# Kernel tuning notes

Hardware: AMD Instinct MI355X
Metric: run time of the kernel (lower is better)

The kernel has to match this reference:

```python
import jax, jax.numpy as jnp
import numpy as np

B, S, D, H = 2, 2048, 1024, 16
HD = D // H  # 64

def setup_inputs() -> dict:
    key = jax.random.key(0)
    ks = jax.random.split(key, 6)
    s = 1.0 / np.sqrt(D)
    return {
        "x": jax.random.normal(ks[0], (B, S, D), dtype=jnp.float32),
        "wq": jax.random.normal(ks[1], (D, D), dtype=jnp.float32) * s,
        "wk": jax.random.normal(ks[2], (D, D), dtype=jnp.float32) * s,
        "wv": jax.random.normal(ks[3], (D, D), dtype=jnp.float32) * s,
        "wo": jax.random.normal(ks[4], (D, D), dtype=jnp.float32) * s,
        "bo": jax.random.normal(ks[5], (D,), dtype=jnp.float32) * 0.01,
    }

def reference(x, wq, wk, wv, wo, bo):
    b, s, _ = x.shape
    # QKV projections (qkvBias=False), reshape to [b, h, s, hd]
    q = (x @ wq).reshape(b, s, H, HD).transpose(0, 2, 1, 3)
    k = (x @ wk).reshape(b, s, H, HD).transpose(0, 2, 1, 3)
    v = (x @ wv).reshape(b, s, H, HD).transpose(0, 2, 1, 3)
    # scores, causal mask (upper triangle -> -inf), scale, softmax
    scores = jnp.einsum('bhqd,bhkd->bhqk', q, k)
    causal = jnp.triu(jnp.ones((s, s), dtype=bool), k=1)
    scores = jnp.where(causal, -jnp.inf, scores) / np.sqrt(HD)
    weights = jax.nn.softmax(scores, axis=-1)  # dropout=0 (eval)
    ctx = jnp.einsum('bhqk,bhkd->bhqd', weights, v)
    ctx = ctx.transpose(0, 2, 1, 3).reshape(b, s, D)
    return ctx @ wo + bo
```

## Files before the change

kernel.cpp:

```cpp
#include <hip/hip_runtime.h>
#include <hip/hip_bf16.h>
#include <math.h>

#define BB 2
#define SS 2048
#define DD 1024
#define HH 16
#define HDIM 64

typedef unsigned short u16;
typedef __attribute__((ext_vector_type(8))) short bfrag;
typedef __attribute__((ext_vector_type(4))) short s16x4;
typedef __attribute__((ext_vector_type(4))) float f32x4;

#define NEG_BIG (-1e30f)
#define QSCALE 0.18033688011112042f

__device__ __forceinline__ u16 f2u(float f) {
    unsigned int u = __builtin_bit_cast(unsigned int, f);
    u += 0x7fffu + ((u >> 16) & 1u);
    return (u16)(u >> 16);
}

__device__ __forceinline__ void async16(const u16* g, u16* l) {
    __builtin_amdgcn_global_load_lds((__attribute__((address_space(1))) void*)g,
                                     (__attribute__((address_space(3))) void*)l,
                                     16, 0, 0);
}

__device__ __forceinline__ f32x4 mfma16(bfrag a, bfrag b, f32x4 c) {
    return __builtin_amdgcn_mfma_f32_16x16x32_bf16(a, b, c, 0, 0, 0);
}

__device__ __forceinline__ f32x4 mfma_pv(s16x4 a, s16x4 b, f32x4 c) {
#if __has_builtin(__builtin_amdgcn_mfma_f32_16x16x16_bf16)
    return __builtin_amdgcn_mfma_f32_16x16x16_bf16(a, b, c, 0, 0, 0);
#elif __has_builtin(__builtin_amdgcn_mfma_f32_16x16x16bf16_1k)
    return __builtin_amdgcn_mfma_f32_16x16x16bf16_1k(a, b, c, 0, 0, 0);
#else
    f32x4 d;
    asm("v_mfma_f32_16x16x16_bf16 %0, %1, %2, %3" : "=v"(d) : "v"(a), "v"(b), "v"(c));
    return d;
#endif
}

__global__ __launch_bounds__(256) void prep_k(
    const float* __restrict__ x,  u16* __restrict__ xb,
    const float* __restrict__ wq, const float* __restrict__ wk,
    const float* __restrict__ wv, const float* __restrict__ wo,
    u16* __restrict__ wT)
{
    const int id = blockIdx.x;
    const int t = threadIdx.x;
    if (id < 2048) {
        int i = (id * 256 + t) * 8;
        float4 a = *(const float4*)(x + i);
        float4 b = *(const float4*)(x + i + 4);
        u16 o[8] = { f2u(a.x), f2u(a.y), f2u(a.z), f2u(a.w),
                     f2u(b.x), f2u(b.y), f2u(b.z), f2u(b.w) };
        *(uint4*)(xb + i) = *(uint4*)o;
        return;
    }
    const int wid = id - 2048;
    const int z = wid >> 8;
    const int kt = wid & 15, nt = (wid >> 4) & 15;
    const float* w = (z == 0) ? wq : (z == 1) ? wk : (z == 2) ? wv : wo;
    u16* o = wT + (size_t)z * DD * DD;
    __shared__ __align__(16) u16 T[64][72];
    const int k0 = kt * 64, n0 = nt * 64;
    {
        int kr = t >> 2, nb = (t & 3) * 16;
        const float4* s4 = (const float4*)(w + (size_t)(k0 + kr) * DD + n0 + nb);
        #pragma unroll
        for (int jj = 0; jj < 4; ++jj) {
            float4 v = s4[jj];
            T[kr][nb + jj*4 + 0] = f2u(v.x);
            T[kr][nb + jj*4 + 1] = f2u(v.y);
            T[kr][nb + jj*4 + 2] = f2u(v.z);
            T[kr][nb + jj*4 + 3] = f2u(v.w);
        }
    }
    __syncthreads();
    {
        int nr = t >> 2, kb = (t & 3) * 16;
        u16 tmp[16];
        #pragma unroll
        for (int j = 0; j < 16; ++j) tmp[j] = T[kb + j][nr];
        *(uint4*)(o + (size_t)(n0 + nr) * DD + k0 + kb)     = ((uint4*)tmp)[0];
        *(uint4*)(o + (size_t)(n0 + nr) * DD + k0 + kb + 8) = ((uint4*)tmp)[1];
    }
}

__global__ __launch_bounds__(256) void gemm_qkv_k(
    const u16* __restrict__ xb, const u16* __restrict__ wT,
    u16* __restrict__ Qo, u16* __restrict__ Ko, u16* __restrict__ Vt)
{
    const u16* wTz = wT + (size_t)blockIdx.z * DD * DD;
    const float osc = (blockIdx.z == 0) ? QSCALE : 1.0f;

    __shared__ __align__(16) u16 As[128 * 64];
    __shared__ __align__(16) u16 Bs[64 * 64];

    const int t = threadIdx.x;
    const int m0 = blockIdx.x * 128, n0 = blockIdx.y * 64;
    const int lane15 = t & 15, quad = (t >> 4) & 3, wave = t >> 6;
    const int wm = wave & 1, wn = wave >> 1;

    int arow[4], acol[4];
    #pragma unroll
    for (int i = 0; i < 4; ++i) {
        int c = t + i * 256;
        arow[i] = c >> 3;
        acol[i] = (c & 7) ^ (arow[i] & 7);
    }
    const int br0 = t >> 3,         bs0 = t & 7;
    const int br1 = (t + 256) >> 3, bs1 = (t + 256) & 7;
    const int bc0 = bs0 ^ (br0 & 7);
    const int bc1 = bs1 ^ (br1 & 7);
    const int ldb = (t & 192) * 8;

    int aoff[4][2], boff[2][2];
    #pragma unroll
    for (int mi = 0; mi < 4; ++mi) {
        int r = wm * 64 + mi * 16 + lane15;
        #pragma unroll
        for (int kh = 0; kh < 2; ++kh)
            aoff[mi][kh] = (r * 8 + ((kh * 4 + quad) ^ (r & 7))) * 8;
    }
    #pragma unroll
    for (int ni = 0; ni < 2; ++ni) {
        int r = wn * 32 + ni * 16 + lane15;
        #pragma unroll
        for (int kh = 0; kh < 2; ++kh)
            boff[ni][kh] = (r * 8 + ((kh * 4 + quad) ^ (r & 7))) * 8;
    }

    f32x4 acc[4][2];
    #pragma unroll
    for (int mi = 0; mi < 4; ++mi)
        #pragma unroll
        for (int ni = 0; ni < 2; ++ni)
            acc[mi][ni] = (f32x4){0.f, 0.f, 0.f, 0.f};

    for (int it = 0; it < 16; ++it) {
        const int k0 = it * 64;
        #pragma unroll
        for (int i = 0; i < 4; ++i)
            async16(xb + (size_t)(m0 + arow[i]) * DD + k0 + acol[i] * 8,
                    As + ldb + i * 2048);
        async16(wTz + (size_t)(n0 + br0) * DD + k0 + bc0 * 8, Bs + ldb);
        async16(wTz + (size_t)(n0 + br1) * DD + k0 + bc1 * 8, Bs + ldb + 2048);
        __syncthreads();
        #pragma unroll
        for (int kh = 0; kh < 2; ++kh) {
            bfrag av[4], bv[2];
            #pragma unroll
            for (int mi = 0; mi < 4; ++mi) av[mi] = *(const bfrag*)(As + aoff[mi][kh]);
            #pragma unroll
            for (int ni = 0; ni < 2; ++ni) bv[ni] = *(const bfrag*)(Bs + boff[ni][kh]);
            #pragma unroll
            for (int mi = 0; mi < 4; ++mi)
                #pragma unroll
                for (int ni = 0; ni < 2; ++ni)
                    acc[mi][ni] = mfma16(av[mi], bv[ni], acc[mi][ni]);
        }
        __syncthreads();
    }

    const int h = n0 >> 6;
    const int bq = m0 >> 11;
    const int ms = m0 & (SS - 1);

    if (blockIdx.z != 2) {
        u16* out = (blockIdx.z == 0) ? Qo : Ko;
        u16* dst = out + (((size_t)(bq * HH + h)) * SS) * HDIM;
        #pragma unroll
        for (int mi = 0; mi < 4; ++mi) {
            #pragma unroll
            for (int r = 0; r < 4; ++r) {
                int s = ms + wm * 64 + mi * 16 + quad * 4 + r;
                #pragma unroll
                for (int ni = 0; ni < 2; ++ni) {
                    int hd = wn * 32 + ni * 16 + lane15;
                    dst[(size_t)s * HDIM + hd] = f2u(acc[mi][ni][r] * osc);
                }
            }
        }
    } else {
        u16* T = As;
        __syncthreads();
        #pragma unroll
        for (int mi = 0; mi < 4; ++mi)
            #pragma unroll
            for (int r = 0; r < 4; ++r) {
                int ml = wm * 64 + mi * 16 + quad * 4 + r;
                #pragma unroll
                for (int ni = 0; ni < 2; ++ni) {
                    int nl = wn * 32 + ni * 16 + lane15;
                    T[nl * 128 + (ml ^ ((nl & 7) << 4))] = f2u(acc[mi][ni][r]);
                }
            }
        __syncthreads();
        u16* dst = Vt + ((size_t)(bq * HH + h)) * (HDIM * SS);
        #pragma unroll
        for (int i = 0; i < 4; ++i) {
            int c = t + i * 256;
            int row = c >> 4;
            int mb  = (c & 15) * 8;
            uint4 val = *(const uint4*)&T[row * 128 + (mb ^ ((row & 7) << 4))];
            *(uint4*)(dst + (size_t)row * SS + ms + mb) = val;
        }
    }
}

__global__ __launch_bounds__(256) void gemm_out_k(
    const u16* __restrict__ ctxb, const u16* __restrict__ woT,
    const float* __restrict__ bo, float* __restrict__ out)
{
    __shared__ __align__(16) u16 As[128 * 64];
    __shared__ __align__(16) u16 Bs[64 * 64];

    const int t = threadIdx.x;
    const int m0 = blockIdx.x * 128, n0 = blockIdx.y * 64;
    const int lane15 = t & 15, quad = (t >> 4) & 3, wave = t >> 6;
    const int wm = wave & 1, wn = wave >> 1;

    int arow[4], acol[4];
    #pragma unroll
    for (int i = 0; i < 4; ++i) {
        int c = t + i * 256;
        arow[i] = c >> 3;
        acol[i] = (c & 7) ^ (arow[i] & 7);
    }
    const int br0 = t >> 3,         bs0 = t & 7;
    const int br1 = (t + 256) >> 3, bs1 = (t + 256) & 7;
    const int bc0 = bs0 ^ (br0 & 7);
    const int bc1 = bs1 ^ (br1 & 7);
    const int ldb = (t & 192) * 8;

    int aoff[4][2], boff[2][2];
    #pragma unroll
    for (int mi = 0; mi < 4; ++mi) {
        int r = wm * 64 + mi * 16 + lane15;
        #pragma unroll
        for (int kh = 0; kh < 2; ++kh)
            aoff[mi][kh] = (r * 8 + ((kh * 4 + quad) ^ (r & 7))) * 8;
    }
    #pragma unroll
    for (int ni = 0; ni < 2; ++ni) {
        int r = wn * 32 + ni * 16 + lane15;
        #pragma unroll
        for (int kh = 0; kh < 2; ++kh)
            boff[ni][kh] = (r * 8 + ((kh * 4 + quad) ^ (r & 7))) * 8;
    }

    f32x4 acc[4][2];
    #pragma unroll
    for (int mi = 0; mi < 4; ++mi)
        #pragma unroll
        for (int ni = 0; ni < 2; ++ni)
            acc[mi][ni] = (f32x4){0.f, 0.f, 0.f, 0.f};

    for (int it = 0; it < 16; ++it) {
        const int k0 = it * 64;
        #pragma unroll
        for (int i = 0; i < 4; ++i)
            async16(ctxb + (size_t)(m0 + arow[i]) * DD + k0 + acol[i] * 8,
                    As + ldb + i * 2048);
        async16(woT + (size_t)(n0 + br0) * DD + k0 + bc0 * 8, Bs + ldb);
        async16(woT + (size_t)(n0 + br1) * DD + k0 + bc1 * 8, Bs + ldb + 2048);
        __syncthreads();
        #pragma unroll
        for (int kh = 0; kh < 2; ++kh) {
            bfrag av[4], bv[2];
            #pragma unroll
            for (int mi = 0; mi < 4; ++mi) av[mi] = *(const bfrag*)(As + aoff[mi][kh]);
            #pragma unroll
            for (int ni = 0; ni < 2; ++ni) bv[ni] = *(const bfrag*)(Bs + boff[ni][kh]);
            #pragma unroll
            for (int mi = 0; mi < 4; ++mi)
                #pragma unroll
                for (int ni = 0; ni < 2; ++ni)
                    acc[mi][ni] = mfma16(av[mi], bv[ni], acc[mi][ni]);
        }
        __syncthreads();
    }

    float bias[2];
    #pragma unroll
    for (int ni = 0; ni < 2; ++ni)
        bias[ni] = bo[n0 + wn * 32 + ni * 16 + lane15];

    #pragma unroll
    for (int mi = 0; mi < 4; ++mi) {
        #pragma unroll
        for (int r = 0; r < 4; ++r) {
            int m = m0 + wm * 64 + mi * 16 + quad * 4 + r;
            #pragma unroll
            for (int ni = 0; ni < 2; ++ni) {
                int n = n0 + wn * 32 + ni * 16 + lane15;
                out[(size_t)m * DD + n] = acc[mi][ni][r] + bias[ni];
            }
        }
    }
}

struct AttnState {
    f32x4 acc_o[4];
    f32x4 acc_s;
};

template<bool MASKED>
__device__ __forceinline__ void qkt_pv(
    const u16* __restrict__ Kc, const u16* __restrict__ Vc,
    const bfrag bq[2], const int koff[2], const int voffb[4],
    bool qhi, int kv0, int qg, int quad4,
    AttnState& st, s16x4 ones4)
{
    f32x4 sT[4];
    #pragma unroll
    for (int ni = 0; ni < 4; ++ni) sT[ni] = (f32x4){0.f, 0.f, 0.f, 0.f};

    bfrag vv[2][4];
    #pragma unroll
    for (int nd = 0; nd < 4; ++nd)
        vv[0][nd] = *(const bfrag*)&Vc[voffb[0] + nd * 1024];

    __builtin_amdgcn_s_setprio(1);
    #pragma unroll
    for (int kh = 0; kh < 2; ++kh)
        #pragma unroll
        for (int ni = 0; ni < 4; ++ni)
            sT[ni] = mfma16(*(const bfrag*)&Kc[koff[kh] + ni * 1024], bq[kh], sT[ni]);
    __builtin_amdgcn_s_setprio(0);

    #pragma unroll
    for (int ni = 0; ni < 4; ++ni) {
        if (ni < 3) {
            #pragma unroll
            for (int nd = 0; nd < 4; ++nd)
                vv[(ni + 1) & 1][nd] = *(const bfrag*)&Vc[voffb[ni + 1] + nd * 1024];
        }
        float pv[4];
        #pragma unroll
        for (int r = 0; r < 4; ++r) {
            float v = sT[ni][r];
            if (MASKED) {
                int kvg = kv0 + ni * 16 + quad4 + r;
                if (kvg > qg) v = NEG_BIG;
            }
            pv[r] = exp2f(v);
        }
        unsigned lo = __builtin_amdgcn_perm(
            __builtin_bit_cast(unsigned, pv[1]),
            __builtin_bit_cast(unsigned, pv[0]), 0x07060302u);
        unsigned hi = __builtin_amdgcn_perm(
            __builtin_bit_cast(unsigned, pv[3]),
            __builtin_bit_cast(unsigned, pv[2]), 0x07060302u);
        s16x4 pf = __builtin_bit_cast(s16x4,
            ((unsigned long long)hi << 32) | (unsigned long long)lo);
        __builtin_amdgcn_s_setprio(1);
        st.acc_s = mfma_pv(ones4, pf, st.acc_s);
        #pragma unroll
        for (int nd = 0; nd < 4; ++nd) {
            bfrag v8 = vv[ni & 1][nd];
            s16x4 vlo = __builtin_shufflevector(v8, v8, 0, 1, 2, 3);
            s16x4 vhi = __builtin_shufflevector(v8, v8, 4, 5, 6, 7);
            s16x4 va = qhi ? vhi : vlo;
            st.acc_o[nd] = mfma_pv(va, pf, st.acc_o[nd]);
        }
        __builtin_amdgcn_s_setprio(0);
    }
}

__global__ __launch_bounds__(256, 4) void attn_k(
    const u16* __restrict__ Q, const u16* __restrict__ K,
    const u16* __restrict__ Vt, u16* __restrict__ ctx)
{
    __shared__ __align__(16) u16 Ks[2][64 * 64];
    __shared__ __align__(16) u16 Vs[2][64 * 64];
    const int t = threadIdx.x;
    const int lane15 = t & 15, quad = (t >> 4) & 3, wave = t >> 6;
    const int bh = blockIdx.x;
    const int yy = (int)blockIdx.y;
    const int y0 = yy & 7, rnd = yy >> 3;
    const int qt = (rnd == 0) ? 31 - y0 : (rnd == 1) ? y0
                 : (rnd == 2) ? 23 - y0 : 8 + y0;
    const int q0 = qt * 64;
    const int b = bh >> 4, h = bh & 15;
    const u16* Qb = Q  + (size_t)bh * SS * HDIM;
    const u16* Kb = K  + (size_t)bh * SS * HDIM;
    const u16* Vb = Vt + (size_t)bh * HDIM * SS;

    const int kr0 = t >> 3,         ks0 = t & 7;
    const int kr1 = (t + 256) >> 3, ks1 = (t + 256) & 7;
    const int kc0 = ks0 ^ (kr0 & 7);
    const int kc1 = ks1 ^ (kr1 & 7);
    const int ldst = (t & 192) * 8;

    async16(Qb + (size_t)(q0 + kr0) * HDIM + kc0 * 8, &Ks[1][ldst]);
    async16(Qb + (size_t)(q0 + kr1) * HDIM + kc1 * 8, &Ks[1][ldst + 2048]);
    async16(Kb + (size_t)kr0 * HDIM + kc0 * 8, &Ks[0][ldst]);
    async16(Kb + (size_t)kr1 * HDIM + kc1 * 8, &Ks[0][ldst + 2048]);
    async16(Vb + (size_t)kr0 * SS + kc0 * 8, &Vs[0][ldst]);
    async16(Vb + (size_t)kr1 * SS + kc1 * 8, &Vs[0][ldst + 2048]);

    const int r7 = lane15 & 7;
    int koff[2];
    #pragma unroll
    for (int kh = 0; kh < 2; ++kh)
        koff[kh] = (lane15 * 8 + ((kh * 4 + quad) ^ r7)) * 8;
    int voffb[4];
    #pragma unroll
    for (int ni = 0; ni < 4; ++ni)
        voffb[ni] = (lane15 * 8 + ((ni * 2 + (quad >> 1)) ^ r7)) * 8;
    const bool qhi = (quad & 1) != 0;

    __syncthreads();
    bfrag bq[2];
    bq[0] = *(const bfrag*)&Ks[1][koff[0] + wave * 1024];
    bq[1] = *(const bfrag*)&Ks[1][koff[1] + wave * 1024];
    __syncthreads();

    s16x4 ones4;
    #pragma unroll
    for (int i = 0; i < 4; ++i) ones4[i] = (short)0x3f80;

    AttnState st;
    st.acc_s = (f32x4){0.f, 0.f, 0.f, 0.f};
    #pragma unroll
    for (int nd = 0; nd < 4; ++nd) st.acc_o[nd] = (f32x4){0.f, 0.f, 0.f, 0.f};

    const int qg = q0 + wave * 16 + lane15;
    const int quad4 = quad * 4;

    for (int kt = 0; kt < qt; ++kt) {
        const int nv0 = (kt + 1) * 64;
        const int pb = (kt + 1) & 1;
        async16(Kb + (size_t)(nv0 + kr0) * HDIM + kc0 * 8, &Ks[pb][ldst]);
        async16(Kb + (size_t)(nv0 + kr1) * HDIM + kc1 * 8, &Ks[pb][ldst + 2048]);
        async16(Vb + (size_t)kr0 * SS + nv0 + kc0 * 8, &Vs[pb][ldst]);
        async16(Vb + (size_t)kr1 * SS + nv0 + kc1 * 8, &Vs[pb][ldst + 2048]);
        qkt_pv<false>(Ks[kt & 1], Vs[kt & 1], bq, koff, voffb,
                      qhi, kt * 64, qg, quad4, st, ones4);
        __syncthreads();
    }
    qkt_pv<true>(Ks[qt & 1], Vs[qt & 1], bq, koff, voffb,
                 qhi, qt * 64, qg, quad4, st, ones4);

    const float inv = 1.f / st.acc_s[0];
    const int srow = q0 + wave * 16 + lane15;
    u16* dst = ctx + ((size_t)b * SS + srow) * DD + h * HDIM + quad4;
    #pragma unroll
    for (int nd = 0; nd < 4; ++nd) {
        uint2 stw;
        stw.x = (unsigned)f2u(st.acc_o[nd][0] * inv) |
                ((unsigned)f2u(st.acc_o[nd][1] * inv) << 16);
        stw.y = (unsigned)f2u(st.acc_o[nd][2] * inv) |
                ((unsigned)f2u(st.acc_o[nd][3] * inv) << 16);
        *(uint2*)(dst + nd * 16) = stw;
    }
}

extern "C" void kernel_launch(void* const* d_in, const int* in_sizes, int n_in,
                              void* d_out, int out_size, void* d_ws, size_t ws_size,
                              hipStream_t stream) {
    const float* x  = (const float*)d_in[0];
    const float* wq = (const float*)d_in[1];
    const float* wk = (const float*)d_in[2];
    const float* wv = (const float*)d_in[3];
    const float* wo = (const float*)d_in[4];
    const float* bo = (const float*)d_in[5];
    float* out = (float*)d_out;

    char* ws = (char*)d_ws;
    const size_t MB8 = (size_t)8 * 1024 * 1024;
    u16* xb  = (u16*)(ws);
    u16* wT  = (u16*)(ws + MB8);
    u16* Qb  = (u16*)(ws + 2 * MB8);
    u16* Kb  = (u16*)(ws + 3 * MB8);
    u16* Vt  = (u16*)(ws + 4 * MB8);
    u16* ctxb = xb;

    prep_k    <<<3072, 256, 0, stream>>>(x, xb, wq, wk, wv, wo, wT);
    gemm_qkv_k<<<dim3(32, 16, 3), 256, 0, stream>>>(xb, wT, Qb, Kb, Vt);
    attn_k    <<<dim3(32, 32), 256, 0, stream>>>(Qb, Kb, Vt, ctxb);
    gemm_out_k<<<dim3(32, 16), 256, 0, stream>>>(ctxb, wT + (size_t)3 * DD * DD, bo, out);
}
```

Measured before the change: 180.6 us.

## Shrink output GEMM tile, slim attention registers, use native exp2

The output projection GEMM moves from 128x64 to 64x64 tiles with a K step of 128, which doubles the grid to 1024 blocks for better CU fill and halves the barriers per K. The attention inner loop drops the double-buffered V register prefetch and instead reads 4-element V fragments directly from LDS at a quad-dependent offset. It also raises the launch-bounds occupancy hint from 4 to 5 and swaps exp2f for the raw hardware exp2 builtin. The loop's global pointers are now incremented rather than recomputed. Risks include more LDS read latency on the critical path in attention and lower per-block reuse in the smaller GEMM tile.

```diff
diff --git a/kernel.cpp b/kernel.cpp
--- a/kernel.cpp
+++ b/kernel.cpp
@@ -20,6 +20,14 @@
     unsigned int u = __builtin_bit_cast(unsigned int, f);
     u += 0x7fffu + ((u >> 16) & 1u);
     return (u16)(u >> 16);
+}
+
+__device__ __forceinline__ float fexp2(float x) {
+#if __has_builtin(__builtin_amdgcn_exp2f)
+    return __builtin_amdgcn_exp2f(x);
+#else
+    return exp2f(x);
+#endif
 }
 
 __device__ __forceinline__ void async16(const u16* g, u16* l) {
@@ -217,31 +225,24 @@
     const u16* __restrict__ ctxb, const u16* __restrict__ woT,
     const float* __restrict__ bo, float* __restrict__ out)
 {
-    __shared__ __align__(16) u16 As[128 * 64];
-    __shared__ __align__(16) u16 Bs[64 * 64];
+    __shared__ __align__(16) u16 As[2][4096];
+    __shared__ __align__(16) u16 Bs[2][4096];
 
     const int t = threadIdx.x;
-    const int m0 = blockIdx.x * 128, n0 = blockIdx.y * 64;
+    const int m0 = blockIdx.x * 64, n0 = blockIdx.y * 64;
     const int lane15 = t & 15, quad = (t >> 4) & 3, wave = t >> 6;
     const int wm = wave & 1, wn = wave >> 1;
 
-    int arow[4], acol[4];
-    #pragma unroll
-    for (int i = 0; i < 4; ++i) {
-        int c = t + i * 256;
-        arow[i] = c >> 3;
-        acol[i] = (c & 7) ^ (arow[i] & 7);
-    }
     const int br0 = t >> 3,         bs0 = t & 7;
     const int br1 = (t + 256) >> 3, bs1 = (t + 256) & 7;
     const int bc0 = bs0 ^ (br0 & 7);
     const int bc1 = bs1 ^ (br1 & 7);
     const int ldb = (t & 192) * 8;
 
-    int aoff[4][2], boff[2][2];
-    #pragma unroll
-    for (int mi = 0; mi < 4; ++mi) {
-        int r = wm * 64 + mi * 16 + lane15;
+    int aoff[2][2], boff[2][2];
+    #pragma unroll
+    for (int mi = 0; mi < 2; ++mi) {
+        int r = wm * 32 + mi * 16 + lane15;
         #pragma unroll
         for (int kh = 0; kh < 2; ++kh)
             aoff[mi][kh] = (r * 8 + ((kh * 4 + quad) ^ (r & 7))) * 8;
@@ -254,34 +255,39 @@
             boff[ni][kh] = (r * 8 + ((kh * 4 + quad) ^ (r & 7))) * 8;
     }
 
-    f32x4 acc[4][2];
-    #pragma unroll
-    for (int mi = 0; mi < 4; ++mi)
+    f32x4 acc[2][2];
+    #pragma unroll
+    for (int mi = 0; mi < 2; ++mi)
         #pragma unroll
         for (int ni = 0; ni < 2; ++ni)
             acc[mi][ni] = (f32x4){0.f, 0.f, 0.f, 0.f};
 
-    for (int it = 0; it < 16; ++it) {
-        const int k0 = it * 64;
-        #pragma unroll
-        for (int i = 0; i < 4; ++i)
-            async16(ctxb + (size_t)(m0 + arow[i]) * DD + k0 + acol[i] * 8,
-                    As + ldb + i * 2048);
-        async16(woT + (size_t)(n0 + br0) * DD + k0 + bc0 * 8, Bs + ldb);
-        async16(woT + (size_t)(n0 + br1) * DD + k0 + bc1 * 8, Bs + ldb + 2048);
-        __syncthreads();
-        #pragma unroll
-        for (int kh = 0; kh < 2; ++kh) {
-            bfrag av[4], bv[2];
-            #pragma unroll
-            for (int mi = 0; mi < 4; ++mi) av[mi] = *(const bfrag*)(As + aoff[mi][kh]);
-            #pragma unroll
-            for (int ni = 0; ni < 2; ++ni) bv[ni] = *(const bfrag*)(Bs + boff[ni][kh]);
-            #pragma unroll
-            for (int mi = 0; mi < 4; ++mi)
-                #pragma unroll
-                for (int ni = 0; ni < 2; ++ni)
-                    acc[mi][ni] = mfma16(av[mi], bv[ni], acc[mi][ni]);
+    for (int it = 0; it < 8; ++it) {
+        const int k0 = it * 128;
+        #pragma unroll
+        for (int hh = 0; hh < 2; ++hh) {
+            const int kh64 = k0 + hh * 64;
+            async16(ctxb + (size_t)(m0 + br0) * DD + kh64 + bc0 * 8, &As[hh][ldb]);
+            async16(ctxb + (size_t)(m0 + br1) * DD + kh64 + bc1 * 8, &As[hh][ldb + 2048]);
+            async16(woT  + (size_t)(n0 + br0) * DD + kh64 + bc0 * 8, &Bs[hh][ldb]);
+            async16(woT  + (size_t)(n0 + br1) * DD + kh64 + bc1 * 8, &Bs[hh][ldb + 2048]);
+        }
+        __syncthreads();
+        #pragma unroll
+        for (int hh = 0; hh < 2; ++hh) {
+            #pragma unroll
+            for (int kh = 0; kh < 2; ++kh) {
+                bfrag av[2], bv[2];
+                #pragma unroll
+                for (int mi = 0; mi < 2; ++mi) av[mi] = *(const bfrag*)&As[hh][aoff[mi][kh]];
+                #pragma unroll
+                for (int ni = 0; ni < 2; ++ni) bv[ni] = *(const bfrag*)&Bs[hh][boff[ni][kh]];
+                #pragma unroll
+                for (int mi = 0; mi < 2; ++mi)
+                    #pragma unroll
+                    for (int ni = 0; ni < 2; ++ni)
+                        acc[mi][ni] = mfma16(av[mi], bv[ni], acc[mi][ni]);
+            }
         }
         __syncthreads();
     }
@@ -292,10 +298,10 @@
         bias[ni] = bo[n0 + wn * 32 + ni * 16 + lane15];
 
     #pragma unroll
-    for (int mi = 0; mi < 4; ++mi) {
+    for (int mi = 0; mi < 2; ++mi) {
         #pragma unroll
         for (int r = 0; r < 4; ++r) {
-            int m = m0 + wm * 64 + mi * 16 + quad * 4 + r;
+            int m = m0 + wm * 32 + mi * 16 + quad * 4 + r;
             #pragma unroll
             for (int ni = 0; ni < 2; ++ni) {
                 int n = n0 + wn * 32 + ni * 16 + lane15;
@@ -305,26 +311,15 @@
     }
 }
 
-struct AttnState {
-    f32x4 acc_o[4];
-    f32x4 acc_s;
-};
-
 template<bool MASKED>
 __device__ __forceinline__ void qkt_pv(
     const u16* __restrict__ Kc, const u16* __restrict__ Vc,
-    const bfrag bq[2], const int koff[2], const int voffb[4],
-    bool qhi, int kv0, int qg, int quad4,
-    AttnState& st, s16x4 ones4)
+    const bfrag bq[2], const int koff[2], const int voff[4],
+    int kv0, int qg, int quad4, f32x4 acc_o[4], f32x4& acc_s, s16x4 ones4)
 {
     f32x4 sT[4];
     #pragma unroll
     for (int ni = 0; ni < 4; ++ni) sT[ni] = (f32x4){0.f, 0.f, 0.f, 0.f};
-
-    bfrag vv[2][4];
-    #pragma unroll
-    for (int nd = 0; nd < 4; ++nd)
-        vv[0][nd] = *(const bfrag*)&Vc[voffb[0] + nd * 1024];
 
     __builtin_amdgcn_s_setprio(1);
     #pragma unroll
@@ -336,11 +331,6 @@
 
     #pragma unroll
     for (int ni = 0; ni < 4; ++ni) {
-        if (ni < 3) {
-            #pragma unroll
-            for (int nd = 0; nd < 4; ++nd)
-                vv[(ni + 1) & 1][nd] = *(const bfrag*)&Vc[voffb[ni + 1] + nd * 1024];
-        }
         float pv[4];
         #pragma unroll
         for (int r = 0; r < 4; ++r) {
@@ -349,7 +339,7 @@
                 int kvg = kv0 + ni * 16 + quad4 + r;
                 if (kvg > qg) v = NEG_BIG;
             }
-            pv[r] = exp2f(v);
+            pv[r] = fexp2(v);
         }
         unsigned lo = __builtin_amdgcn_perm(
             __builtin_bit_cast(unsigned, pv[1]),
@@ -360,20 +350,16 @@
         s16x4 pf = __builtin_bit_cast(s16x4,
             ((unsigned long long)hi << 32) | (unsigned long long)lo);
         __builtin_amdgcn_s_setprio(1);
-        st.acc_s = mfma_pv(ones4, pf, st.acc_s);
-        #pragma unroll
-        for (int nd = 0; nd < 4; ++nd) {
-            bfrag v8 = vv[ni & 1][nd];
-            s16x4 vlo = __builtin_shufflevector(v8, v8, 0, 1, 2, 3);
-            s16x4 vhi = __builtin_shufflevector(v8, v8, 4, 5, 6, 7);
-            s16x4 va = qhi ? vhi : vlo;
-            st.acc_o[nd] = mfma_pv(va, pf, st.acc_o[nd]);
-        }
+        acc_s = mfma_pv(ones4, pf, acc_s);
+        #pragma unroll
+        for (int nd = 0; nd < 4; ++nd)
+            acc_o[nd] = mfma_pv(*(const s16x4*)&Vc[voff[ni] + nd * 1024],
+                                pf, acc_o[nd]);
         __builtin_amdgcn_s_setprio(0);
     }
 }
 
-__global__ __launch_bounds__(256, 4) void attn_k(
+__global__ __launch_bounds__(256, 5) void attn_k(
     const u16* __restrict__ Q, const u16* __restrict__ K,
     const u16* __restrict__ Vt, u16* __restrict__ ctx)
 {
@@ -398,23 +384,27 @@
     const int kc1 = ks1 ^ (kr1 & 7);
     const int ldst = (t & 192) * 8;
 
+    const u16* kga = Kb + (size_t)kr0 * HDIM + kc0 * 8;
+    const u16* kgb = Kb + (size_t)kr1 * HDIM + kc1 * 8;
+    const u16* vga = Vb + (size_t)kr0 * SS + kc0 * 8;
+    const u16* vgb = Vb + (size_t)kr1 * SS + kc1 * 8;
+
     async16(Qb + (size_t)(q0 + kr0) * HDIM + kc0 * 8, &Ks[1][ldst]);
     async16(Qb + (size_t)(q0 + kr1) * HDIM + kc1 * 8, &Ks[1][ldst + 2048]);
-    async16(Kb + (size_t)kr0 * HDIM + kc0 * 8, &Ks[0][ldst]);
-    async16(Kb + (size_t)kr1 * HDIM + kc1 * 8, &Ks[0][ldst + 2048]);
-    async16(Vb + (size_t)kr0 * SS + kc0 * 8, &Vs[0][ldst]);
-    async16(Vb + (size_t)kr1 * SS + kc1 * 8, &Vs[0][ldst + 2048]);
+    async16(kga, &Ks[0][ldst]);
+    async16(kgb, &Ks[0][ldst + 2048]);
+    async16(vga, &Vs[0][ldst]);
+    async16(vgb, &Vs[0][ldst + 2048]);
 
     const int r7 = lane15 & 7;
     int koff[2];
     #pragma unroll
     for (int kh = 0; kh < 2; ++kh)
         koff[kh] = (lane15 * 8 + ((kh * 4 + quad) ^ r7)) * 8;
-    int voffb[4];
+    int voff[4];
     #pragma unroll
     for (int ni = 0; ni < 4; ++ni)
-        voffb[ni] = (lane15 * 8 + ((ni * 2 + (quad >> 1)) ^ r7)) * 8;
-    const bool qhi = (quad & 1) != 0;
+        voff[ni] = (lane15 * 8 + ((ni * 2 + (quad >> 1)) ^ r7)) * 8 + (quad & 1) * 4;
 
     __syncthreads();
     bfrag bq[2];
@@ -426,38 +416,44 @@
     #pragma unroll
     for (int i = 0; i < 4; ++i) ones4[i] = (short)0x3f80;
 
-    AttnState st;
-    st.acc_s = (f32x4){0.f, 0.f, 0.f, 0.f};
-    #pragma unroll
-    for (int nd = 0; nd < 4; ++nd) st.acc_o[nd] = (f32x4){0.f, 0.f, 0.f, 0.f};
+    f32x4 acc_o[4];
+    f32x4 acc_s = (f32x4){0.f, 0.f, 0.f, 0.f};
+    #pragma unroll
+    for (int nd = 0; nd < 4; ++nd) acc_o[nd] = (f32x4){0.f, 0.f, 0.f, 0.f};
 
     const int qg = q0 + wave * 16 + lane15;
     const int quad4 = quad * 4;
 
+    const u16* kpa = kga + 64 * HDIM;
+    const u16* kpb = kgb + 64 * HDIM;
+    const u16* vpa = vga + 64;
+    const u16* vpb = vgb + 64;
+
     for (int kt = 0; kt < qt; ++kt) {
-        const int nv0 = (kt + 1) * 64;
         const int pb = (kt + 1) & 1;
-        async16(Kb + (size_t)(nv0 + kr0) * HDIM + kc0 * 8, &Ks[pb][ldst]);
-        async16(Kb + (size_t)(nv0 + kr1) * HDIM + kc1 * 8, &Ks[pb][ldst + 2048]);
-        async16(Vb + (size_t)kr0 * SS + nv0 + kc0 * 8, &Vs[pb][ldst]);
-        async16(Vb + (size_t)kr1 * SS + nv0 + kc1 * 8, &Vs[pb][ldst + 2048]);
-        qkt_pv<false>(Ks[kt & 1], Vs[kt & 1], bq, koff, voffb,
-                      qhi, kt * 64, qg, quad4, st, ones4);
-        __syncthreads();
-    }
-    qkt_pv<true>(Ks[qt & 1], Vs[qt & 1], bq, koff, voffb,
-                 qhi, qt * 64, qg, quad4, st, ones4);
-
-    const float inv = 1.f / st.acc_s[0];
+        async16(kpa, &Ks[pb][ldst]);
+        async16(kpb, &Ks[pb][ldst + 2048]);
+        async16(vpa, &Vs[pb][ldst]);
+        async16(vpb, &Vs[pb][ldst + 2048]);
+        kpa += 64 * HDIM; kpb += 64 * HDIM;
+        vpa += 64;        vpb += 64;
+        qkt_pv<false>(Ks[kt & 1], Vs[kt & 1], bq, koff, voff,
+                      kt * 64, qg, quad4, acc_o, acc_s, ones4);
+        __syncthreads();
+    }
+    qkt_pv<true>(Ks[qt & 1], Vs[qt & 1], bq, koff, voff,
+                 qt * 64, qg, quad4, acc_o, acc_s, ones4);
+
+    const float inv = 1.f / acc_s[0];
     const int srow = q0 + wave * 16 + lane15;
     u16* dst = ctx + ((size_t)b * SS + srow) * DD + h * HDIM + quad4;
     #pragma unroll
     for (int nd = 0; nd < 4; ++nd) {
         uint2 stw;
-        stw.x = (unsigned)f2u(st.acc_o[nd][0] * inv) |
-                ((unsigned)f2u(st.acc_o[nd][1] * inv) << 16);
-        stw.y = (unsigned)f2u(st.acc_o[nd][2] * inv) |
-                ((unsigned)f2u(st.acc_o[nd][3] * inv) << 16);
+        stw.x = (unsigned)f2u(acc_o[nd][0] * inv) |
+                ((unsigned)f2u(acc_o[nd][1] * inv) << 16);
+        stw.y = (unsigned)f2u(acc_o[nd][2] * inv) |
+                ((unsigned)f2u(acc_o[nd][3] * inv) << 16);
         *(uint2*)(dst + nd * 16) = stw;
     }
 }
@@ -485,5 +481,5 @@
     prep_k    <<<3072, 256, 0, stream>>>(x, xb, wq, wk, wv, wo, wT);
     gemm_qkv_k<<<dim3(32, 16, 3), 256, 0, stream>>>(xb, wT, Qb, Kb, Vt);
     attn_k    <<<dim3(32, 32), 256, 0, stream>>>(Qb, Kb, Vt, ctxb);
-    gemm_out_k<<<dim3(32, 16), 256, 0, stream>>>(ctxb, wT + (size_t)3 * DD * DD, bo, out);
-}
+    gemm_out_k<<<dim3(64, 16), 256, 0, stream>>>(ctxb, wT + (size_t)3 * DD * DD, bo, out);
+}
```

Measured after the change: 169.6 us. -6.1%, faster.
